# Kernel tuning notes

Hardware: AMD Instinct MI355X
Metric: run time of the kernel (lower is better)

## Reference

```python
import jax, jax.numpy as jnp
import numpy as np

N, E, D_IN, H, OUT = 50000, 800000, 128, 256, 2
BN_EPS = 1e-5
LN_EPS = 1e-5


def _xavier(k, fi, fo):
    lim = float(np.sqrt(6.0 / (fi + fo)))
    return jax.random.uniform(k, (fi, fo), minval=-lim, maxval=lim, dtype=jnp.float32)


def setup_inputs() -> dict:
    key = jax.random.key(0)
    ks = jax.random.split(key, 8)
    return {
        "x": jax.random.normal(ks[0], (N, D_IN), dtype=jnp.float32),
        "edge_index": jax.random.randint(ks[1], (2, E), 0, N, dtype=jnp.int32),
        "feature_scale": jnp.ones((D_IN,), jnp.float32),
        "feature_bias": jnp.zeros((D_IN,), jnp.float32),
        "bn0_g": jnp.ones((D_IN,), jnp.float32),
        "bn0_b": jnp.zeros((D_IN,), jnp.float32),
        "W1": _xavier(ks[2], D_IN, H), "b1": jnp.zeros((H,), jnp.float32),
        "bn1_g": jnp.ones((H,), jnp.float32), "bn1_b": jnp.zeros((H,), jnp.float32),
        "ln1_g": jnp.ones((H,), jnp.float32), "ln1_b": jnp.zeros((H,), jnp.float32),
        "W2": _xavier(ks[3], H, H), "b2": jnp.zeros((H,), jnp.float32),
        "bn2_g": jnp.ones((H,), jnp.float32), "bn2_b": jnp.zeros((H,), jnp.float32),
        "ln2_g": jnp.ones((H,), jnp.float32), "ln2_b": jnp.zeros((H,), jnp.float32),
        "Wout": _xavier(ks[4], H, OUT), "bout": jnp.zeros((OUT,), jnp.float32),
    }


def _batchnorm(x, g, b):
    # training-mode BatchNorm1d: batch stats over node axis, biased variance
    mu = jnp.mean(x, axis=0)
    var = jnp.mean(jnp.square(x - mu), axis=0)
    return g * (x - mu) * jax.lax.rsqrt(var + BN_EPS) + b


def _layernorm(x, g, b):
    mu = jnp.mean(x, axis=-1, keepdims=True)
    var = jnp.mean(jnp.square(x - mu), axis=-1, keepdims=True)
    return g * (x - mu) * jax.lax.rsqrt(var + LN_EPS) + b


def _gcn(x, W, b, src, dst, dinv):
    # PyG GCNConv with self-loops: D^{-1/2}(A+I)D^{-1/2} X W + b
    h = x @ W                                   # [N, F]
    norm = (dinv[src] * dinv[dst])[:, None]     # [E, 1]
    msg = h[src] * norm                         # [E, F] (dominant traffic)
    agg = jax.ops.segment_sum(msg, dst, num_segments=N)
    return agg + (dinv * dinv)[:, None] * h + b


def _forward(x, feature_scale, feature_bias, bn0_g, bn0_b,
             W1, b1, bn1_g, bn1_b, ln1_g, ln1_b,
             W2, b2, bn2_g, bn2_b, ln2_g, ln2_b,
             Wout, bout, edge_index):
    src, dst = edge_index[0], edge_index[1]
    deg = jax.ops.segment_sum(jnp.ones((E,), x.dtype), dst, num_segments=N) + 1.0
    dinv = jax.lax.rsqrt(deg)

    h = x * feature_scale + feature_bias
    h = _batchnorm(h, bn0_g, bn0_b)            # input_bn; dropout = identity (eval)

    # layer 0 (no residual: i == 0)
    h1 = _gcn(h, W1, b1, src, dst, dinv)
    h1 = jax.nn.relu(h1)
    h1 = _batchnorm(h1, bn1_g, bn1_b)
    h1 = _layernorm(h1, ln1_g, ln1_b)

    # layer 1 (residual add, shapes match)
    h2 = _gcn(h1, W2, b2, src, dst, dinv)
    h2 = jax.nn.relu(h2)
    h2 = _batchnorm(h2, bn2_g, bn2_b)
    h2 = _layernorm(h2, ln2_g, ln2_b)
    h2 = h2 + h1

    return h2 @ Wout + bout


def reference(x, edge_index, feature_scale, feature_bias, bn0_g, bn0_b,
              W1, b1, bn1_g, bn1_b, ln1_g, ln1_b,
              W2, b2, bn2_g, bn2_b, ln2_g, ln2_b,
              Wout, bout):
    return _forward(x, feature_scale, feature_bias, bn0_g, bn0_b,
                    W1, b1, bn1_g, bn1_b, ln1_g, ln1_b,
                    W2, b2, bn2_g, bn2_b, ln2_g, ln2_b,
                    Wout, bout, edge_index)
```

## Files before the change

### kernel.cpp

```cpp
#include <hip/hip_runtime.h>
#include <hip/hip_bf16.h>
#include <stdint.h>

#define N_NODES 50000
#define N_EDGES 800000
#define D_IN    128
#define H_DIM   256
#define BN_EPS  1e-5f
#define LN_EPS  1e-5f
#define NBLK_SCAN 196
#define NBLK_HIST 32
#define NBLK2 1563
#define SLICE_ELEMS ((size_t)N_NODES * 32)
#define EDGE_CHUNK 3072
#define DEG_BLOCKS 3125
#define BN0_BLOCKS 128
#define PREPX_BLOCKS 6250
#define TR_BLOCKS 256

typedef float v4f __attribute__((ext_vector_type(4)));
typedef short v8s __attribute__((ext_vector_type(8)));

__device__ __forceinline__ float bflo(unsigned u){ return __uint_as_float(u << 16); }
__device__ __forceinline__ float bfhi(unsigned u){ return __uint_as_float(u & 0xffff0000u); }
__device__ __forceinline__ unsigned short f2bf(float f){
  unsigned u = __float_as_uint(f);
  u += 0x7fffu + ((u >> 16) & 1u);
  return (unsigned short)(u >> 16);
}
__device__ __forceinline__ unsigned pack2(float a, float b){
  return (unsigned)f2bf(a) | ((unsigned)f2bf(b) << 16);
}
__device__ __forceinline__ float wred(float v){
  #pragma unroll
  for (int m = 1; m < 64; m <<= 1) v += __shfl_xor(v, m, 64);
  return v;
}

__device__ __forceinline__ int block_excl_scan(int v){
  int t = threadIdx.x;
  int lane = t & 63, w = t >> 6;
  int inc = v;
  #pragma unroll
  for (int m = 1; m < 64; m <<= 1){
    int o = __shfl_up(inc, m, 64);
    if (lane >= m) inc += o;
  }
  __shared__ int wsum[4];
  if (lane == 63) wsum[w] = inc;
  __syncthreads();
  int base = 0;
  #pragma unroll
  for (int j = 0; j < 4; ++j) if (j < w) base += wsum[j];
  return base + inc - v;
}

__global__ __launch_bounds__(256) void degbn_k(const int* ei, const float* x,
                                               const float* fs, const float* fb,
                                               int* cnt, float* S, float* Q){
  int b = blockIdx.x, t = threadIdx.x;
  if (b >= BN0_BLOCKS){
    int e = (b - BN0_BLOCKS) * 256 + t;
    if (e < N_EDGES) atomicAdd(&cnt[ei[N_EDGES + e]], 1);
    return;
  }
  int cl = t & 31, rg = t >> 5;
  int c = cl * 4;
  float4 fs4 = *(const float4*)(fs + c);
  float4 fb4 = *(const float4*)(fb + c);
  float s0=0,s1=0,s2=0,s3=0,q0=0,q1=0,q2=0,q3=0;
  for (int row = b * 8 + rg; row < N_NODES; row += BN0_BLOCKS * 8){
    float4 xv = *(const float4*)(x + (size_t)row * D_IN + c);
    float v0 = xv.x * fs4.x + fb4.x;
    float v1 = xv.y * fs4.y + fb4.y;
    float v2 = xv.z * fs4.z + fb4.z;
    float v3 = xv.w * fs4.w + fb4.w;
    s0 += v0; s1 += v1; s2 += v2; s3 += v3;
    q0 += v0*v0; q1 += v1*v1; q2 += v2*v2; q3 += v3*v3;
  }
  __shared__ float red[256][8];
  red[t][0]=s0; red[t][1]=s1; red[t][2]=s2; red[t][3]=s3;
  red[t][4]=q0; red[t][5]=q1; red[t][6]=q2; red[t][7]=q3;
  __syncthreads();
  float* Sr = S + (b & 3) * D_IN;
  float* Qr = Q + (b & 3) * D_IN;
  if (t < 32){
    float a[8];
    #pragma unroll
    for (int i = 0; i < 8; ++i) a[i] = red[t][i];
    for (int j = 1; j < 8; ++j)
      #pragma unroll
      for (int i = 0; i < 8; ++i) a[i] += red[t + 32*j][i];
    #pragma unroll
    for (int i = 0; i < 4; ++i){ atomicAdd(&Sr[t*4+i], a[i]); atomicAdd(&Qr[t*4+i], a[4+i]); }
  }
}

__global__ __launch_bounds__(256) void hist_k(const int* cnt, int* dhist){
  __shared__ int lh[64];
  int t = threadIdx.x;
  if (t < 64) lh[t] = 0;
  __syncthreads();
  for (int i = blockIdx.x * 256 + t; i < N_NODES; i += NBLK_HIST * 256)
    atomicAdd(&lh[min(cnt[i], 63)], 1);
  __syncthreads();
  if (t < 64 && lh[t] > 0) atomicAdd(&dhist[t], lh[t]);
}

__global__ __launch_bounds__(256) void dperm_k(const int* cnt, const int* dhist, int* reserve,
                                               int* perm, int* rank){
  __shared__ int ep_s[64];
  __shared__ int lh[64], lb[64], lc[64];
  int t = threadIdx.x;
  if (t < 64){
    int v = dhist[t];
    int inc = v;
    #pragma unroll
    for (int m = 1; m < 64; m <<= 1){
      int o = __shfl_up(inc, m, 64);
      if (t >= m) inc += o;
    }
    ep_s[t] = inc - v;
    lh[t] = 0; lc[t] = 0;
  }
  __syncthreads();
  for (int i = blockIdx.x * 256 + t; i < N_NODES; i += NBLK_HIST * 256)
    atomicAdd(&lh[min(cnt[i], 63)], 1);
  __syncthreads();
  if (t < 64 && lh[t] > 0) lb[t] = ep_s[t] + atomicAdd(&reserve[t], lh[t]);
  __syncthreads();
  for (int i = blockIdx.x * 256 + t; i < N_NODES; i += NBLK_HIST * 256){
    int b = min(cnt[i], 63);
    int r = atomicAdd(&lc[b], 1);
    int pos = lb[b] + r;
    perm[pos] = i;
    rank[i] = pos;
  }
}

__global__ __launch_bounds__(256) void blocksum_k(const int* cnt, const int* perm, int* bsum){
  int i = blockIdx.x * 256 + threadIdx.x;
  int v = (i < N_NODES) ? cnt[perm[i]] : 0;
  #pragma unroll
  for (int m = 1; m < 64; m <<= 1) v += __shfl_xor(v, m, 64);
  __shared__ int ws[4];
  int t = threadIdx.x;
  if ((t & 63) == 0) ws[t >> 6] = v;
  __syncthreads();
  if (t == 0) bsum[blockIdx.x] = ws[0] + ws[1] + ws[2] + ws[3];
}

__global__ __launch_bounds__(256) void bscan_k(const int* bsum, int* bpre, int* offs){
  int t = threadIdx.x;
  int v = (t < NBLK_SCAN) ? bsum[t] : 0;
  int e = block_excl_scan(v);
  if (t < NBLK_SCAN) bpre[t] = e;
  if (t == 0) offs[N_NODES] = N_EDGES;
}

__global__ __launch_bounds__(256) void cscan_k(const int* cnt, const int* perm, const int* bpre,
                                               int* offs, int* curs, float* dinv){
  int t = threadIdx.x;
  int i = blockIdx.x * 256 + t;
  int node = 0, v = 0;
  if (i < N_NODES){ node = perm[i]; v = cnt[node]; }
  int e = block_excl_scan(v) + bpre[blockIdx.x];
  if (i < N_NODES){
    offs[i] = e; curs[i] = e;
    dinv[node] = rsqrtf((float)v + 1.0f);
  }
}

__global__ __launch_bounds__(256) void csrprep_k(const int* ei, const int* rank, int* cursor,
                                                 unsigned short* edges,
                                                 const float* x, const float* S, const float* Q,
                                                 const float* fs, const float* fb,
                                                 const float* gg, const float* bb,
                                                 unsigned short* xt,
                                                 const float* W1, const float* W2,
                                                 unsigned short* W1t, unsigned short* W2t){
  int b = blockIdx.x, t = threadIdx.x;
  if (b < DEG_BLOCKS){
    int e = b * 256 + t;
    if (e < N_EDGES){
      int s = ei[e], d = ei[N_EDGES + e];
      int p = atomicAdd(&cursor[rank[d]], 1);
      edges[p] = (unsigned short)s;
    }
    return;
  }
  if (b < DEG_BLOCKS + PREPX_BLOCKS){
    int i = (b - DEG_BLOCKS) * 256 + t;
    int row = i >> 5; int c = (i & 31) * 4;
    float4 Sv = *(const float4*)(S + c);
    float4 Qv = *(const float4*)(Q + c);
    #pragma unroll
    for (int rep = 1; rep < 4; ++rep){
      float4 s2 = *(const float4*)(S + rep * D_IN + c);
      float4 q2 = *(const float4*)(Q + rep * D_IN + c);
      Sv.x += s2.x; Sv.y += s2.y; Sv.z += s2.z; Sv.w += s2.w;
      Qv.x += q2.x; Qv.y += q2.y; Qv.z += q2.z; Qv.w += q2.w;
    }
    float4 fs4 = *(const float4*)(fs + c);
    float4 fb4 = *(const float4*)(fb + c);
    float4 gg4 = *(const float4*)(gg + c);
    float4 bb4 = *(const float4*)(bb + c);
    const float invN = 1.0f / N_NODES;
    float mu0 = Sv.x*invN, mu1 = Sv.y*invN, mu2 = Sv.z*invN, mu3 = Sv.w*invN;
    float r0 = rsqrtf(Qv.x*invN - mu0*mu0 + BN_EPS);
    float r1 = rsqrtf(Qv.y*invN - mu1*mu1 + BN_EPS);
    float r2 = rsqrtf(Qv.z*invN - mu2*mu2 + BN_EPS);
    float r3 = rsqrtf(Qv.w*invN - mu3*mu3 + BN_EPS);
    float a0 = gg4.x*r0*fs4.x, c0 = gg4.x*r0*(fb4.x - mu0) + bb4.x;
    float a1 = gg4.y*r1*fs4.y, c1 = gg4.y*r1*(fb4.y - mu1) + bb4.y;
    float a2 = gg4.z*r2*fs4.z, c2 = gg4.z*r2*(fb4.z - mu2) + bb4.z;
    float a3 = gg4.w*r3*fs4.w, c3 = gg4.w*r3*(fb4.w - mu3) + bb4.w;
    float4 xv = *(const float4*)(x + (size_t)row * D_IN + c);
    uint2 o;
    o.x = pack2(a0 * xv.x + c0, a1 * xv.y + c1);
    o.y = pack2(a2 * xv.z + c2, a3 * xv.w + c3);
    *(uint2*)(xt + (size_t)row * D_IN + c) = o;
    return;
  }
  int i = (b - DEG_BLOCKS - PREPX_BLOCKS) * 256 + t;
  if (i < D_IN * H_DIM){
    int r = i / H_DIM, c = i % H_DIM;
    W1t[c * D_IN + r] = f2bf(W1[i]);
  }
  if (i < H_DIM * H_DIM){
    int r = i / H_DIM, c = i % H_DIM;
    W2t[c * H_DIM + r] = f2bf(W2[i]);
  }
}

template<int K>
__global__ __launch_bounds__(256) void gemm_k(const unsigned short* A, const unsigned short* Bt,
                                              const float* dinv, unsigned short* C, int M){
  __shared__ __align__(16) short smem[16896];
  __shared__ float dvs[64];
  short* As = smem;
  short* Bs = smem + 64 * 40;
  int t = threadIdx.x;
  int m0 = blockIdx.x * 64;
  int lane = t & 63;
  int w = t >> 6;
  int fr = lane & 15, quad = lane >> 4;
  if (t < 64) dvs[t] = (m0 + t < M) ? dinv[m0 + t] : 0.0f;
  v4f acc[4][4] = {};
  int sr = t >> 2;
  int sk = (t & 3) << 3;
  for (int k0 = 0; k0 < K; k0 += 32){
    __syncthreads();
    uint4 av = {0,0,0,0};
    int arow = m0 + sr;
    if (arow < M) av = *(const uint4*)(A + (size_t)arow * K + k0 + sk);
    *(uint4*)(&As[sr * 40 + sk]) = av;
    #pragma unroll
    for (int j = 0; j < 4; ++j){
      int brow = sr + 64 * j;
      uint4 bv = *(const uint4*)(Bt + (size_t)brow * K + k0 + sk);
      *(uint4*)(&Bs[brow * 40 + sk]) = bv;
    }
    __syncthreads();
    v8s af[4], bf[4];
    #pragma unroll
    for (int mi = 0; mi < 4; ++mi)
      af[mi] = *(const v8s*)(&As[(mi * 16 + fr) * 40 + quad * 8]);
    #pragma unroll
    for (int ni = 0; ni < 4; ++ni)
      bf[ni] = *(const v8s*)(&Bs[(w * 64 + ni * 16 + fr) * 40 + quad * 8]);
    #pragma unroll
    for (int mi = 0; mi < 4; ++mi)
      #pragma unroll
      for (int ni = 0; ni < 4; ++ni)
        acc[mi][ni] = __builtin_amdgcn_mfma_f32_16x16x32_bf16(af[mi], bf[ni], acc[mi][ni], 0, 0, 0);
  }
  __syncthreads();
  short* Cs = smem;
  #pragma unroll
  for (int mi = 0; mi < 4; ++mi)
    #pragma unroll
    for (int ni = 0; ni < 4; ++ni)
      #pragma unroll
      for (int r = 0; r < 4; ++r){
        int row = mi * 16 + quad * 4 + r;
        int col = w * 64 + ni * 16 + fr;
        Cs[row * 264 + col] = (short)f2bf(acc[mi][ni][r] * dvs[row]);
      }
  __syncthreads();
  int orow = t >> 2;
  int grow = m0 + orow;
  if (grow < M){
    #pragma unroll
    for (int j = 0; j < 4; ++j){
      int oc = (t & 3) * 16 + 64 * j;
      v8s v0 = *(const v8s*)(&Cs[orow * 264 + oc]);
      v8s v1 = *(const v8s*)(&Cs[orow * 264 + oc + 8]);
      *(v8s*)(&C[(size_t)(oc >> 5) * SLICE_ELEMS + (size_t)grow * 32 + (oc & 31)]) = v0;
      int oc1 = oc + 8;
      *(v8s*)(&C[(size_t)(oc1 >> 5) * SLICE_ELEMS + (size_t)grow * 32 + (oc1 & 31)]) = v1;
    }
  }
}

__global__ __launch_bounds__(256) void agg_k(const unsigned short* hs, const int* offsets,
                                             const unsigned short* edges, const int* perm,
                                             const float* dinv, const float* bias,
                                             unsigned short* g, float* pS, float* pQ){
  __shared__ unsigned eds32[EDGE_CHUNK / 2];
  __shared__ float wps[4][8][8];
  int t = threadIdx.x;
  int lane = t & 63;
  int wv = t >> 6;
  int slice = blockIdx.x & 7;
  int l8 = lane & 7;
  int nb = (blockIdx.x >> 3) * 32;
  int idx = nb + (t >> 3);
  int lastn = min(nb + 32, N_NODES);
  int blk0 = offsets[nb];
  int base = blk0 & ~1;
  int blkN = offsets[lastn];
  const unsigned* gsrc = (const unsigned*)(edges + base);
  int nu = min((blkN - base + 1) >> 1, EDGE_CHUNK / 2);
  for (int i = t; i < nu; i += 256)
    eds32[i] = gsrc[i];
  __syncthreads();
  bool act = idx < N_NODES;
  int node = act ? perm[idx] : 0;
  const unsigned short* hb = hs + (size_t)slice * SLICE_ELEMS;
  float4 bb = *(const float4*)(bias + slice * 32 + l8 * 4);
  uint2 sv = *(const uint2*)(hb + (size_t)node * 32 + l8 * 4);
  float a0 = bflo(sv.x), a1 = bfhi(sv.x);
  float a2 = bflo(sv.y), a3 = bfhi(sv.y);
  int e  = act ? offsets[idx] : 0;
  int e1 = act ? offsets[idx + 1] : 0;
  if ((e & 1) && e < e1){
    int ru = (e - base) >> 1;
    unsigned d = (ru < EDGE_CHUNK / 2) ? eds32[ru] : gsrc[ru];
    unsigned s = d >> 16;
    uint2 v = *(const uint2*)(hb + (size_t)s * 32 + l8 * 4);
    a0 += bflo(v.x); a1 += bfhi(v.x);
    a2 += bflo(v.y); a3 += bfhi(v.y);
    ++e;
  }
  for (; e + 16 <= e1; e += 16){
    int ru = (e - base) >> 1;
    unsigned dd[8];
    if (ru + 8 <= EDGE_CHUNK / 2){
      #pragma unroll
      for (int j = 0; j < 8; ++j) dd[j] = eds32[ru + j];
    } else {
      #pragma unroll
      for (int j = 0; j < 8; ++j) dd[j] = gsrc[ru + j];
    }
    uint2 v[16];
    #pragma unroll
    for (int j = 0; j < 8; ++j){
      v[2*j]   = *(const uint2*)(hb + (size_t)(dd[j] & 0xffffu) * 32 + l8 * 4);
      v[2*j+1] = *(const uint2*)(hb + (size_t)(dd[j] >> 16)     * 32 + l8 * 4);
    }
    #pragma unroll
    for (int j = 0; j < 16; ++j){
      a0 += bflo(v[j].x); a1 += bfhi(v[j].x);
      a2 += bflo(v[j].y); a3 += bfhi(v[j].y);
    }
  }
  if (e + 8 <= e1){
    int ru = (e - base) >> 1;
    unsigned dd[4];
    if (ru + 4 <= EDGE_CHUNK / 2){
      #pragma unroll
      for (int j = 0; j < 4; ++j) dd[j] = eds32[ru + j];
    } else {
      #pragma unroll
      for (int j = 0; j < 4; ++j) dd[j] = gsrc[ru + j];
    }
    uint2 v[8];
    #pragma unroll
    for (int j = 0; j < 4; ++j){
      v[2*j]   = *(const uint2*)(hb + (size_t)(dd[j] & 0xffffu) * 32 + l8 * 4);
      v[2*j+1] = *(const uint2*)(hb + (size_t)(dd[j] >> 16)     * 32 + l8 * 4);
    }
    #pragma unroll
    for (int j = 0; j < 8; ++j){
      a0 += bflo(v[j].x); a1 += bfhi(v[j].x);
      a2 += bflo(v[j].y); a3 += bfhi(v[j].y);
    }
    e += 8;
  }
  for (; e < e1; ++e){
    int r = e - base;
    unsigned d = ((r >> 1) < EDGE_CHUNK / 2) ? eds32[r >> 1] : gsrc[r >> 1];
    unsigned s = (r & 1) ? (d >> 16) : (d & 0xffffu);
    uint2 v = *(const uint2*)(hb + (size_t)s * 32 + l8 * 4);
    a0 += bflo(v.x); a1 += bfhi(v.x);
    a2 += bflo(v.y); a3 += bfhi(v.y);
  }
  float dv = dinv[node];
  float y0 = act ? fmaxf(dv * a0 + bb.x, 0.f) : 0.f;
  float y1 = act ? fmaxf(dv * a1 + bb.y, 0.f) : 0.f;
  float y2 = act ? fmaxf(dv * a2 + bb.z, 0.f) : 0.f;
  float y3 = act ? fmaxf(dv * a3 + bb.w, 0.f) : 0.f;
  if (act){
    uint2 o;
    o.x = pack2(y0, y1); o.y = pack2(y2, y3);
    *(uint2*)(g + (size_t)node * H_DIM + slice * 32 + l8 * 4) = o;
  }
  float q0 = y0*y0, q1 = y1*y1, q2 = y2*y2, q3 = y3*y3;
  #pragma unroll
  for (int m = 8; m < 64; m <<= 1){
    y0 += __shfl_xor(y0, m, 64); y1 += __shfl_xor(y1, m, 64);
    y2 += __shfl_xor(y2, m, 64); y3 += __shfl_xor(y3, m, 64);
    q0 += __shfl_xor(q0, m, 64); q1 += __shfl_xor(q1, m, 64);
    q2 += __shfl_xor(q2, m, 64); q3 += __shfl_xor(q3, m, 64);
  }
  if (lane < 8){
    wps[wv][l8][0] = y0; wps[wv][l8][1] = y1; wps[wv][l8][2] = y2; wps[wv][l8][3] = y3;
    wps[wv][l8][4] = q0; wps[wv][l8][5] = q1; wps[wv][l8][6] = q2; wps[wv][l8][7] = q3;
  }
  __syncthreads();
  if (t < 64){
    int tl8 = t >> 3, ti = t & 7;
    float v = wps[0][tl8][ti] + wps[1][tl8][ti] + wps[2][tl8][ti] + wps[3][tl8][ti];
    int col32 = tl8 * 4 + (ti & 3);
    if (ti < 4) pS[(size_t)blockIdx.x * 32 + col32] = v;
    else        pQ[(size_t)blockIdx.x * 32 + col32] = v;
  }
}

__global__ __launch_bounds__(1024) void redu_k(const float* pS, const float* pQ,
                                               const float* gg, const float* bb,
                                               float* sc, float* sh){
  __shared__ float ls[32][32], lq[32][32];
  int t = threadIdx.x;
  int slice = blockIdx.x;
  int grp = t >> 5, c32 = t & 31;
  float as = 0.f, aq = 0.f;
  for (int blk2 = grp; blk2 < NBLK2; blk2 += 32){
    size_t o = ((size_t)blk2 * 8 + slice) * 32 + c32;
    as += pS[o]; aq += pQ[o];
  }
  ls[grp][c32] = as; lq[grp][c32] = aq;
  __syncthreads();
  if (t < 32){
    float S = 0.f, Q = 0.f;
    #pragma unroll
    for (int gI = 0; gI < 32; ++gI){ S += ls[gI][t]; Q += lq[gI][t]; }
    int col = slice * 32 + t;
    const float invN = 1.0f / N_NODES;
    float mu = S * invN;
    float rs = rsqrtf(Q * invN - mu * mu + BN_EPS);
    float s = gg[col] * rs;
    sc[col] = s;
    sh[col] = bb[col] - s * mu;
  }
}

__global__ __launch_bounds__(256) void apply1_k(const unsigned short* g, const float* sc, const float* sh,
                                                const float* lng, const float* lnb, unsigned short* h1){
  int lane = threadIdx.x & 63;
  int row = blockIdx.x * 4 + (threadIdx.x >> 6);
  if (row >= N_NODES) return;
  int c = lane * 4;
  float4 s4 = *(const float4*)(sc + c);
  float4 h4 = *(const float4*)(sh + c);
  uint2 u = *(const uint2*)(g + (size_t)row * H_DIM + c);
  float v0 = s4.x * bflo(u.x) + h4.x;
  float v1 = s4.y * bfhi(u.x) + h4.y;
  float v2 = s4.z * bflo(u.y) + h4.z;
  float v3 = s4.w * bfhi(u.y) + h4.w;
  float sum = wred(v0 + v1 + v2 + v3);
  float sq  = wred(v0*v0 + v1*v1 + v2*v2 + v3*v3);
  float mu = sum * (1.0f / H_DIM);
  float var = sq * (1.0f / H_DIM) - mu * mu;
  float rs = rsqrtf(var + LN_EPS);
  float4 g4 = *(const float4*)(lng + c);
  float4 b4 = *(const float4*)(lnb + c);
  float y0 = g4.x * (v0 - mu) * rs + b4.x;
  float y1 = g4.y * (v1 - mu) * rs + b4.y;
  float y2 = g4.z * (v2 - mu) * rs + b4.z;
  float y3 = g4.w * (v3 - mu) * rs + b4.w;
  uint2 o; o.x = pack2(y0, y1); o.y = pack2(y2, y3);
  *(uint2*)(h1 + (size_t)row * H_DIM + c) = o;
}

__global__ __launch_bounds__(256) void apply2_k(const unsigned short* g, const float* sc, const float* sh,
                                                const float* lng, const float* lnb,
                                                const unsigned short* h1, const float* Wout,
                                                const float* bout, float* out){
  int lane = threadIdx.x & 63;
  int row = blockIdx.x * 4 + (threadIdx.x >> 6);
  if (row >= N_NODES) return;
  int c = lane * 4;
  float4 s4 = *(const float4*)(sc + c);
  float4 h4 = *(const float4*)(sh + c);
  uint2 u = *(const uint2*)(g + (size_t)row * H_DIM + c);
  float v0 = s4.x * bflo(u.x) + h4.x;
  float v1 = s4.y * bfhi(u.x) + h4.y;
  float v2 = s4.z * bflo(u.y) + h4.z;
  float v3 = s4.w * bfhi(u.y) + h4.w;
  float sum = wred(v0 + v1 + v2 + v3);
  float sq  = wred(v0*v0 + v1*v1 + v2*v2 + v3*v3);
  float mu = sum * (1.0f / H_DIM);
  float var = sq * (1.0f / H_DIM) - mu * mu;
  float rs = rsqrtf(var + LN_EPS);
  float4 g4 = *(const float4*)(lng + c);
  float4 b4 = *(const float4*)(lnb + c);
  uint2 hr = *(const uint2*)(h1 + (size_t)row * H_DIM + c);
  float y0 = g4.x * (v0 - mu) * rs + b4.x + bflo(hr.x);
  float y1 = g4.y * (v1 - mu) * rs + b4.y + bfhi(hr.x);
  float y2 = g4.z * (v2 - mu) * rs + b4.z + bflo(hr.y);
  float y3 = g4.w * (v3 - mu) * rs + b4.w + bfhi(hr.y);
  float4 w0 = *(const float4*)(Wout + c * 2);
  float4 w1 = *(const float4*)(Wout + c * 2 + 4);
  float o0 = y0 * w0.x + y1 * w0.z + y2 * w1.x + y3 * w1.z;
  float o1 = y0 * w0.y + y1 * w0.w + y2 * w1.y + y3 * w1.w;
  o0 = wred(o0); o1 = wred(o1);
  if (lane == 0){
    out[(size_t)row * 2 + 0] = o0 + bout[0];
    out[(size_t)row * 2 + 1] = o1 + bout[1];
  }
}

extern "C" void kernel_launch(void* const* d_in, const int* in_sizes, int n_in,
                              void* d_out, int out_size, void* d_ws, size_t ws_size,
                              hipStream_t stream) {
  const float* x    = (const float*)d_in[0];
  const int*   ei   = (const int*)d_in[1];
  const float* fs   = (const float*)d_in[2];
  const float* fb   = (const float*)d_in[3];
  const float* bn0g = (const float*)d_in[4];
  const float* bn0b = (const float*)d_in[5];
  const float* W1   = (const float*)d_in[6];
  const float* b1   = (const float*)d_in[7];
  const float* bn1g = (const float*)d_in[8];
  const float* bn1b = (const float*)d_in[9];
  const float* ln1g = (const float*)d_in[10];
  const float* ln1b = (const float*)d_in[11];
  const float* W2   = (const float*)d_in[12];
  const float* b2   = (const float*)d_in[13];
  const float* bn2g = (const float*)d_in[14];
  const float* bn2b = (const float*)d_in[15];
  const float* ln2g = (const float*)d_in[16];
  const float* ln2b = (const float*)d_in[17];
  const float* Wout = (const float*)d_in[18];
  const float* bout = (const float*)d_in[19];
  float* out = (float*)d_out;

  char* w = (char*)d_ws;
  int*   cnt   = (int*)(w + 0);
  float* bn0S  = (float*)(w + 200000);
  float* bn0Q  = (float*)(w + 202048);
  float* sc1   = (float*)(w + 204096);
  float* sh1   = (float*)(w + 205120);
  float* sc2   = (float*)(w + 206144);
  float* sh2   = (float*)(w + 207168);
  int*   dhist = (int*)(w + 208192);
  int*   reserve = (int*)(w + 208448);
  const size_t ZERO_BYTES = 208704;
  int*   bsum  = (int*)(w + 208704);
  int*   bpre  = (int*)(w + 209728);
  float* dinv  = (float*)(w + 210752);
  int*   offs  = (int*)(w + 410752);
  int*   curs  = (int*)(w + 610816);
  int*   perm  = (int*)(w + 810816);
  int*   rank  = (int*)(w + 1010816);
  unsigned short* edges = (unsigned short*)(w + 1210880);
  unsigned short* xt   = (unsigned short*)(w + 2810944);
  unsigned short* W1t  = (unsigned short*)(w + 15610944);
  unsigned short* W2t  = (unsigned short*)(w + 15676480);
  unsigned short* hlin = (unsigned short*)(w + 15807552);
  unsigned short* gbuf = (unsigned short*)(w + 41407552);
  unsigned short* h1   = (unsigned short*)(w + 67007552);
  float* pS    = (float*)(w + 92607552);
  float* pQ    = (float*)(w + 94208064);

  (void)in_sizes; (void)n_in; (void)out_size; (void)ws_size;

  hipMemsetAsync(d_ws, 0, ZERO_BYTES, stream);

  degbn_k<<<BN0_BLOCKS + DEG_BLOCKS, 256, 0, stream>>>(ei, x, fs, fb, cnt, bn0S, bn0Q);
  hist_k<<<NBLK_HIST, 256, 0, stream>>>(cnt, dhist);
  dperm_k<<<NBLK_HIST, 256, 0, stream>>>(cnt, dhist, reserve, perm, rank);
  blocksum_k<<<NBLK_SCAN, 256, 0, stream>>>(cnt, perm, bsum);
  bscan_k<<<1, 256, 0, stream>>>(bsum, bpre, offs);
  cscan_k<<<NBLK_SCAN, 256, 0, stream>>>(cnt, perm, bpre, offs, curs, dinv);
  csrprep_k<<<DEG_BLOCKS + PREPX_BLOCKS + TR_BLOCKS, 256, 0, stream>>>(
      ei, rank, curs, edges, x, bn0S, bn0Q, fs, fb, bn0g, bn0b, xt, W1, W2, W1t, W2t);

  int ggrid = (N_NODES + 63) / 64;
  int agg_blocks = NBLK2 * 8;

  gemm_k<D_IN><<<ggrid, 256, 0, stream>>>(xt, W1t, dinv, hlin, N_NODES);
  agg_k<<<agg_blocks, 256, 0, stream>>>(hlin, offs, edges, perm, dinv, b1, gbuf, pS, pQ);
  redu_k<<<8, 1024, 0, stream>>>(pS, pQ, bn1g, bn1b, sc1, sh1);
  apply1_k<<<(N_NODES + 3) / 4, 256, 0, stream>>>(gbuf, sc1, sh1, ln1g, ln1b, h1);

  gemm_k<H_DIM><<<ggrid, 256, 0, stream>>>(h1, W2t, dinv, hlin, N_NODES);
  agg_k<<<agg_blocks, 256, 0, stream>>>(hlin, offs, edges, perm, dinv, b2, gbuf, pS, pQ);
  redu_k<<<8, 1024, 0, stream>>>(pS, pQ, bn2g, bn2b, sc2, sh2);
  apply2_k<<<(N_NODES + 3) / 4, 256, 0, stream>>>(gbuf, sc2, sh2, ln2g, ln2b, h1, Wout, bout, out);
}
```

Baseline: 413.0 us.

## Build CSR via two-pass bucketed radix sort instead of global atomics

Result: faster. 371.0 us (-10.1%).

```diff
diff --git a/kernel.cpp b/kernel.cpp
--- a/kernel.cpp
+++ b/kernel.cpp
@@ -8,15 +8,15 @@
 #define H_DIM   256
 #define BN_EPS  1e-5f
 #define LN_EPS  1e-5f
-#define NBLK_SCAN 196
-#define NBLK_HIST 32
 #define NBLK2 1563
 #define SLICE_ELEMS ((size_t)N_NODES * 32)
 #define EDGE_CHUNK 3072
-#define DEG_BLOCKS 3125
-#define BN0_BLOCKS 128
+#define BN0_BLOCKS 256
 #define PREPX_BLOCKS 6250
 #define TR_BLOCKS 256
+#define NBKT 196
+#define CHUNK 4096
+#define RCHUNKS 196
 
 typedef float v4f __attribute__((ext_vector_type(4)));
 typedef short v8s __attribute__((ext_vector_type(8)));
@@ -55,13 +55,21 @@
   return base + inc - v;
 }
 
-__global__ __launch_bounds__(256) void degbn_k(const int* ei, const float* x,
+__global__ __launch_bounds__(256) void bn0r1_k(const int* ei, const float* x,
                                                const float* fs, const float* fb,
-                                               int* cnt, float* S, float* Q){
+                                               float* S, float* Q, int* ghist){
   int b = blockIdx.x, t = threadIdx.x;
   if (b >= BN0_BLOCKS){
-    int e = (b - BN0_BLOCKS) * 256 + t;
-    if (e < N_EDGES) atomicAdd(&cnt[ei[N_EDGES + e]], 1);
+    __shared__ int lh[NBKT];
+    int b2 = b - BN0_BLOCKS;
+    for (int i = t; i < NBKT; i += 256) lh[i] = 0;
+    __syncthreads();
+    int e0 = b2 * CHUNK;
+    int n = min(CHUNK, N_EDGES - e0);
+    for (int i = t; i < n; i += 256)
+      atomicAdd(&lh[ei[N_EDGES + e0 + i] >> 8], 1);
+    __syncthreads();
+    if (t < NBKT && lh[t] > 0) atomicAdd(&ghist[t], lh[t]);
     return;
   }
   int cl = t & 31, rg = t >> 5;
@@ -96,101 +104,116 @@
   }
 }
 
-__global__ __launch_bounds__(256) void hist_k(const int* cnt, int* dhist){
-  __shared__ int lh[64];
+__global__ __launch_bounds__(256) void scanb_k(const int* ghist, int* gcursor, int* bbase){
   int t = threadIdx.x;
-  if (t < 64) lh[t] = 0;
-  __syncthreads();
-  for (int i = blockIdx.x * 256 + t; i < N_NODES; i += NBLK_HIST * 256)
-    atomicAdd(&lh[min(cnt[i], 63)], 1);
-  __syncthreads();
-  if (t < 64 && lh[t] > 0) atomicAdd(&dhist[t], lh[t]);
-}
-
-__global__ __launch_bounds__(256) void dperm_k(const int* cnt, const int* dhist, int* reserve,
-                                               int* perm, int* rank){
-  __shared__ int ep_s[64];
-  __shared__ int lh[64], lb[64], lc[64];
+  int v = (t < NBKT) ? ghist[t] : 0;
+  int e = block_excl_scan(v);
+  if (t < NBKT){ gcursor[t] = e; bbase[t] = e; }
+  if (t == 0) bbase[NBKT] = N_EDGES;
+}
+
+__global__ __launch_bounds__(256) void r3_k(const int* ei, int* gcursor, unsigned* ebuf){
+  __shared__ unsigned short dstS[CHUNK];
+  __shared__ int lh[NBKT], cb[NBKT];
   int t = threadIdx.x;
-  if (t < 64){
-    int v = dhist[t];
-    int inc = v;
-    #pragma unroll
-    for (int m = 1; m < 64; m <<= 1){
-      int o = __shfl_up(inc, m, 64);
-      if (t >= m) inc += o;
-    }
-    ep_s[t] = inc - v;
-    lh[t] = 0; lc[t] = 0;
-  }
-  __syncthreads();
-  for (int i = blockIdx.x * 256 + t; i < N_NODES; i += NBLK_HIST * 256)
-    atomicAdd(&lh[min(cnt[i], 63)], 1);
-  __syncthreads();
-  if (t < 64 && lh[t] > 0) lb[t] = ep_s[t] + atomicAdd(&reserve[t], lh[t]);
-  __syncthreads();
-  for (int i = blockIdx.x * 256 + t; i < N_NODES; i += NBLK_HIST * 256){
-    int b = min(cnt[i], 63);
+  int e0 = blockIdx.x * CHUNK;
+  int n = min(CHUNK, N_EDGES - e0);
+  for (int i = t; i < NBKT; i += 256) lh[i] = 0;
+  __syncthreads();
+  for (int i = t; i < n; i += 256){
+    int d = ei[N_EDGES + e0 + i];
+    dstS[i] = (unsigned short)d;
+    atomicAdd(&lh[d >> 8], 1);
+  }
+  __syncthreads();
+  if (t < NBKT && lh[t] > 0) cb[t] = atomicAdd(&gcursor[t], lh[t]);
+  __syncthreads();
+  if (t < NBKT) lh[t] = 0;
+  __syncthreads();
+  for (int i = t; i < n; i += 256){
+    int d = dstS[i];
+    int bkt = d >> 8;
+    int r = atomicAdd(&lh[bkt], 1);
+    unsigned src = (unsigned)ei[e0 + i];
+    ebuf[cb[bkt] + r] = ((unsigned)(d & 255) << 16) | src;
+  }
+}
+
+__global__ __launch_bounds__(256) void r4a_k(const unsigned* ebuf, const int* bbase,
+                                             int* cnt, int* dhist){
+  __shared__ int h[256], dh[128];
+  int t = threadIdx.x, b = blockIdx.x;
+  h[t] = 0;
+  if (t < 128) dh[t] = 0;
+  __syncthreads();
+  int lo = bbase[b], hi = bbase[b + 1];
+  for (int i = lo + t; i < hi; i += 256)
+    atomicAdd(&h[(ebuf[i] >> 16) & 255], 1);
+  __syncthreads();
+  int node = b * 256 + t;
+  if (node < N_NODES){
+    cnt[node] = h[t];
+    atomicAdd(&dh[min(h[t], 127)], 1);
+  }
+  __syncthreads();
+  if (t < 128 && dh[t] > 0) atomicAdd(&dhist[t], dh[t]);
+}
+
+__global__ __launch_bounds__(256) void dperm2_k(const int* cnt, const int* dhist, int* reserve,
+                                                int* perm, int* rank, int* offs, float* dinv){
+  __shared__ int ep_s[128], W_s[128], lb[128], lh[128], lc[128];
+  int t = threadIdx.x;
+  int v = (t < 128) ? dhist[t] : 0;
+  int e1 = block_excl_scan(v);
+  __syncthreads();
+  int e2 = block_excl_scan((t < 128) ? v * t : 0);
+  __syncthreads();
+  if (t < 128){ ep_s[t] = e1; W_s[t] = e2; lh[t] = 0; lc[t] = 0; }
+  __syncthreads();
+  for (int i = blockIdx.x * 256 + t; i < N_NODES; i += 32 * 256)
+    atomicAdd(&lh[min(cnt[i], 127)], 1);
+  __syncthreads();
+  if (t < 128 && lh[t] > 0) lb[t] = ep_s[t] + atomicAdd(&reserve[t], lh[t]);
+  __syncthreads();
+  for (int i = blockIdx.x * 256 + t; i < N_NODES; i += 32 * 256){
+    int d = cnt[i];
+    int b = min(d, 127);
     int r = atomicAdd(&lc[b], 1);
     int pos = lb[b] + r;
     perm[pos] = i;
     rank[i] = pos;
-  }
-}
-
-__global__ __launch_bounds__(256) void blocksum_k(const int* cnt, const int* perm, int* bsum){
-  int i = blockIdx.x * 256 + threadIdx.x;
-  int v = (i < N_NODES) ? cnt[perm[i]] : 0;
-  #pragma unroll
-  for (int m = 1; m < 64; m <<= 1) v += __shfl_xor(v, m, 64);
-  __shared__ int ws[4];
-  int t = threadIdx.x;
-  if ((t & 63) == 0) ws[t >> 6] = v;
-  __syncthreads();
-  if (t == 0) bsum[blockIdx.x] = ws[0] + ws[1] + ws[2] + ws[3];
-}
-
-__global__ __launch_bounds__(256) void bscan_k(const int* bsum, int* bpre, int* offs){
-  int t = threadIdx.x;
-  int v = (t < NBLK_SCAN) ? bsum[t] : 0;
-  int e = block_excl_scan(v);
-  if (t < NBLK_SCAN) bpre[t] = e;
-  if (t == 0) offs[N_NODES] = N_EDGES;
-}
-
-__global__ __launch_bounds__(256) void cscan_k(const int* cnt, const int* perm, const int* bpre,
-                                               int* offs, int* curs, float* dinv){
-  int t = threadIdx.x;
-  int i = blockIdx.x * 256 + t;
-  int node = 0, v = 0;
-  if (i < N_NODES){ node = perm[i]; v = cnt[node]; }
-  int e = block_excl_scan(v) + bpre[blockIdx.x];
-  if (i < N_NODES){
-    offs[i] = e; curs[i] = e;
-    dinv[node] = rsqrtf((float)v + 1.0f);
-  }
-}
-
-__global__ __launch_bounds__(256) void csrprep_k(const int* ei, const int* rank, int* cursor,
-                                                 unsigned short* edges,
-                                                 const float* x, const float* S, const float* Q,
-                                                 const float* fs, const float* fb,
-                                                 const float* gg, const float* bb,
-                                                 unsigned short* xt,
-                                                 const float* W1, const float* W2,
-                                                 unsigned short* W1t, unsigned short* W2t){
+    offs[pos] = W_s[b] + (pos - ep_s[b]) * d;
+    dinv[i] = rsqrtf((float)d + 1.0f);
+  }
+  if (blockIdx.x == 0 && t == 0) offs[N_NODES] = N_EDGES;
+}
+
+__global__ __launch_bounds__(256) void r4b_k(const unsigned* ebuf, const int* bbase,
+                                             const int* rank, const int* offs,
+                                             unsigned short* edges){
+  __shared__ int curs[256];
+  int t = threadIdx.x, b = blockIdx.x;
+  int node = b * 256 + t;
+  if (node < N_NODES) curs[t] = offs[rank[node]];
+  __syncthreads();
+  int lo = bbase[b], hi = bbase[b + 1];
+  for (int i = lo + t; i < hi; i += 256){
+    unsigned u = ebuf[i];
+    int l8 = (u >> 16) & 255;
+    int pos = atomicAdd(&curs[l8], 1);
+    edges[pos] = (unsigned short)(u & 0xffffu);
+  }
+}
+
+__global__ __launch_bounds__(256) void prep_k(const float* x, const float* S, const float* Q,
+                                              const float* fs, const float* fb,
+                                              const float* gg, const float* bb,
+                                              unsigned short* xt,
+                                              const float* W1, const float* W2,
+                                              unsigned short* W1t, unsigned short* W2t){
   int b = blockIdx.x, t = threadIdx.x;
-  if (b < DEG_BLOCKS){
-    int e = b * 256 + t;
-    if (e < N_EDGES){
-      int s = ei[e], d = ei[N_EDGES + e];
-      int p = atomicAdd(&cursor[rank[d]], 1);
-      edges[p] = (unsigned short)s;
-    }
-    return;
-  }
-  if (b < DEG_BLOCKS + PREPX_BLOCKS){
-    int i = (b - DEG_BLOCKS) * 256 + t;
+  if (b < PREPX_BLOCKS){
+    int i = b * 256 + t;
     int row = i >> 5; int c = (i & 31) * 4;
     float4 Sv = *(const float4*)(S + c);
     float4 Qv = *(const float4*)(Q + c);
@@ -222,7 +245,7 @@
     *(uint2*)(xt + (size_t)row * D_IN + c) = o;
     return;
   }
-  int i = (b - DEG_BLOCKS - PREPX_BLOCKS) * 256 + t;
+  int i = (b - PREPX_BLOCKS) * 256 + t;
   if (i < D_IN * H_DIM){
     int r = i / H_DIM, c = i % H_DIM;
     W1t[c * D_IN + r] = f2bf(W1[i]);
@@ -548,45 +571,46 @@
   float* out = (float*)d_out;
 
   char* w = (char*)d_ws;
-  int*   cnt   = (int*)(w + 0);
-  float* bn0S  = (float*)(w + 200000);
-  float* bn0Q  = (float*)(w + 202048);
-  float* sc1   = (float*)(w + 204096);
-  float* sh1   = (float*)(w + 205120);
-  float* sc2   = (float*)(w + 206144);
-  float* sh2   = (float*)(w + 207168);
-  int*   dhist = (int*)(w + 208192);
-  int*   reserve = (int*)(w + 208448);
-  const size_t ZERO_BYTES = 208704;
-  int*   bsum  = (int*)(w + 208704);
-  int*   bpre  = (int*)(w + 209728);
-  float* dinv  = (float*)(w + 210752);
-  int*   offs  = (int*)(w + 410752);
-  int*   curs  = (int*)(w + 610816);
-  int*   perm  = (int*)(w + 810816);
-  int*   rank  = (int*)(w + 1010816);
-  unsigned short* edges = (unsigned short*)(w + 1210880);
-  unsigned short* xt   = (unsigned short*)(w + 2810944);
-  unsigned short* W1t  = (unsigned short*)(w + 15610944);
-  unsigned short* W2t  = (unsigned short*)(w + 15676480);
-  unsigned short* hlin = (unsigned short*)(w + 15807552);
-  unsigned short* gbuf = (unsigned short*)(w + 41407552);
-  unsigned short* h1   = (unsigned short*)(w + 67007552);
-  float* pS    = (float*)(w + 92607552);
-  float* pQ    = (float*)(w + 94208064);
+  float* bn0S  = (float*)(w + 0);
+  float* bn0Q  = (float*)(w + 2048);
+  int*   dhist = (int*)(w + 4096);
+  int*   reserve = (int*)(w + 4608);
+  int*   ghist  = (int*)(w + 5120);
+  int*   gcursor= (int*)(w + 5904);
+  const size_t ZERO_BYTES = 6688;
+  int*   bbase  = (int*)(w + 6688);
+  float* sc1   = (float*)(w + 7488);
+  float* sh1   = (float*)(w + 8512);
+  float* sc2   = (float*)(w + 9536);
+  float* sh2   = (float*)(w + 10560);
+  int*   cnt   = (int*)(w + 11584);
+  float* dinv  = (float*)(w + 211584);
+  int*   offs  = (int*)(w + 411584);
+  int*   perm  = (int*)(w + 611712);
+  int*   rank  = (int*)(w + 811712);
+  unsigned short* edges = (unsigned short*)(w + 1011712);
+  unsigned short* xt   = (unsigned short*)(w + 2611712);
+  unsigned short* W1t  = (unsigned short*)(w + 15411712);
+  unsigned short* W2t  = (unsigned short*)(w + 15477248);
+  unsigned short* hlin = (unsigned short*)(w + 15608320);
+  unsigned*       ebuf = (unsigned*)(w + 15608320);
+  unsigned short* gbuf = (unsigned short*)(w + 41208320);
+  unsigned short* h1   = (unsigned short*)(w + 66808320);
+  float* pS    = (float*)(w + 92408320);
+  float* pQ    = (float*)(w + 94008832);
 
   (void)in_sizes; (void)n_in; (void)out_size; (void)ws_size;
 
   hipMemsetAsync(d_ws, 0, ZERO_BYTES, stream);
 
-  degbn_k<<<BN0_BLOCKS + DEG_BLOCKS, 256, 0, stream>>>(ei, x, fs, fb, cnt, bn0S, bn0Q);
-  hist_k<<<NBLK_HIST, 256, 0, stream>>>(cnt, dhist);
-  dperm_k<<<NBLK_HIST, 256, 0, stream>>>(cnt, dhist, reserve, perm, rank);
-  blocksum_k<<<NBLK_SCAN, 256, 0, stream>>>(cnt, perm, bsum);
-  bscan_k<<<1, 256, 0, stream>>>(bsum, bpre, offs);
-  cscan_k<<<NBLK_SCAN, 256, 0, stream>>>(cnt, perm, bpre, offs, curs, dinv);
-  csrprep_k<<<DEG_BLOCKS + PREPX_BLOCKS + TR_BLOCKS, 256, 0, stream>>>(
-      ei, rank, curs, edges, x, bn0S, bn0Q, fs, fb, bn0g, bn0b, xt, W1, W2, W1t, W2t);
+  bn0r1_k<<<BN0_BLOCKS + RCHUNKS, 256, 0, stream>>>(ei, x, fs, fb, bn0S, bn0Q, ghist);
+  scanb_k<<<1, 256, 0, stream>>>(ghist, gcursor, bbase);
+  r3_k<<<RCHUNKS, 256, 0, stream>>>(ei, gcursor, ebuf);
+  r4a_k<<<NBKT, 256, 0, stream>>>(ebuf, bbase, cnt, dhist);
+  dperm2_k<<<32, 256, 0, stream>>>(cnt, dhist, reserve, perm, rank, offs, dinv);
+  r4b_k<<<NBKT, 256, 0, stream>>>(ebuf, bbase, rank, offs, edges);
+  prep_k<<<PREPX_BLOCKS + TR_BLOCKS, 256, 0, stream>>>(x, bn0S, bn0Q, fs, fb, bn0g, bn0b,
+                                                       xt, W1, W2, W1t, W2t);
 
   int ggrid = (N_NODES + 63) / 64;
   int agg_blocks = NBLK2 * 8;
```
